# Optimization experiments

Hardware: AMD Instinct MI355X
Metric: run time of the kernel (lower is better)

Reference implementation:

```python
import jax, jax.numpy as jnp
import numpy as np

# longformer-base-4096 config
L, H, D, DH, FF = 12, 12, 768, 64, 3072
B, S, W = 1, 4096, 256            # W = one-sided attention window (attention_window 512)
V, MAXP, NCLS = 50265, 4098, 6
NC = S // W                        # number of chunks of size W


def layer_norm(x, s, b, eps=1e-5):
    m = jnp.mean(x, -1, keepdims=True)
    v = jnp.var(x, -1, keepdims=True)
    return (x - m) * jax.lax.rsqrt(v + eps) * s + b


def sliding_attn(q, k, v, kv_mask):
    # q,k,v: [B,H,S,DH]; kv_mask: [B,S] float (1=keep, 0=pad)
    qc = q.reshape(B, H, NC, W, DH)
    pad = ((0, 0), (0, 0), (W, W), (0, 0))
    kp = jnp.pad(k, pad).reshape(B, H, NC + 2, W, DH)
    vp = jnp.pad(v, pad).reshape(B, H, NC + 2, W, DH)
    # each chunk c sees key chunks c-1, c, c+1 -> [B,H,NC,3W,DH]
    k3 = jnp.concatenate([kp[:, :, i:i + NC] for i in range(3)], axis=3)
    v3 = jnp.concatenate([vp[:, :, i:i + NC] for i in range(3)], axis=3)
    scores = jnp.einsum('bhcqd,bhckd->bhcqk', qc, k3) / np.float32(np.sqrt(DH))
    # banded mask: |key_global - query_global| <= W  <=>  qi <= kj <= qi + 2W
    qi = jnp.arange(W)[:, None]
    kj = jnp.arange(3 * W)[None, :]
    band = (kj >= qi) & (kj <= qi + 2 * W)                       # [W,3W]
    mp = jnp.pad(kv_mask, ((0, 0), (W, W))).reshape(B, NC + 2, W)
    m3 = jnp.concatenate([mp[:, i:i + NC] for i in range(3)], axis=2)  # [B,NC,3W]
    allowed = band[None, None, None] & (m3[:, None, :, None, :] > 0)
    probs = jax.nn.softmax(jnp.where(allowed, scores, -1e9), axis=-1)
    out = jnp.einsum('bhcqk,bhckd->bhcqd', probs, v3)            # [B,H,NC,W,DH]
    return out.reshape(B, H, S, DH)


def setup_inputs():
    ki = iter(jax.random.split(jax.random.key(0), 16))
    p = lambda sh: 0.02 * jax.random.normal(next(ki), sh, jnp.float32)
    ids = jax.random.randint(next(ki), (B, S), 0, V, dtype=jnp.int32)
    mask = jnp.ones((B, S), jnp.int32)
    return dict(
        ids=ids, mask=mask,
        word_emb=p((V, D)), pos_emb=p((MAXP, D)), type_emb=p((D,)),
        ln_e_s=jnp.ones((D,), jnp.float32), ln_e_b=jnp.zeros((D,), jnp.float32),
        wq=p((L, D, D)), bq=jnp.zeros((L, D), jnp.float32),
        wk=p((L, D, D)), bk=jnp.zeros((L, D), jnp.float32),
        wv=p((L, D, D)), bv=jnp.zeros((L, D), jnp.float32),
        wo=p((L, D, D)), bo=jnp.zeros((L, D), jnp.float32),
        ln1_s=jnp.ones((L, D), jnp.float32), ln1_b=jnp.zeros((L, D), jnp.float32),
        w1=p((L, D, FF)), b1=jnp.zeros((L, FF), jnp.float32),
        w2=p((L, FF, D)), b2=jnp.zeros((L, D), jnp.float32),
        ln2_s=jnp.ones((L, D), jnp.float32), ln2_b=jnp.zeros((L, D), jnp.float32),
        w_pool=p((D, D)), b_pool=jnp.zeros((D,), jnp.float32),
        w_cls=p((D, NCLS)), b_cls=jnp.zeros((NCLS,), jnp.float32))


def reference(ids, mask, word_emb, pos_emb, type_emb, ln_e_s, ln_e_b,
              wq, bq, wk, bk, wv, bv, wo, bo, ln1_s, ln1_b,
              w1, b1, w2, b2, ln2_s, ln2_b, w_pool, b_pool, w_cls, b_cls):
    maskf = mask.astype(jnp.float32)
    # RoBERTa-style position ids with padding_idx=1
    pos = (jnp.cumsum(mask, axis=1) * mask + 1).astype(jnp.int32)
    x = word_emb[ids] + pos_emb[pos] + type_emb               # [B,S,D]
    x = layer_norm(x, ln_e_s, ln_e_b)

    def heads(y, w, b):
        return (y @ w + b).reshape(B, S, H, DH).transpose(0, 2, 1, 3)

    for l in range(L):
        q = heads(x, wq[l], bq[l])
        k = heads(x, wk[l], bk[l])
        v = heads(x, wv[l], bv[l])
        a = sliding_attn(q, k, v, maskf)                      # [B,H,S,DH]
        a = a.transpose(0, 2, 1, 3).reshape(B, S, D)
        x = layer_norm(x + (a @ wo[l] + bo[l]), ln1_s[l], ln1_b[l])
        h = jax.nn.gelu(x @ w1[l] + b1[l], approximate=False)
        x = layer_norm(x + (h @ w2[l] + b2[l]), ln2_s[l], ln2_b[l])

    pooled = jnp.tanh(x[:, 0] @ w_pool + b_pool)              # [B,D] pooler
    # Dropout(0.3) is identity in eval mode
    return pooled @ w_cls + b_cls                             # [B,6]
```

## Files before the change

### kernel.cpp

```cpp
#include <hip/hip_runtime.h>
#include <stdint.h>
#include <math.h>

#define NL 12
#define SQ 4096
#define DM 768
#define NH 12
#define DHD 64
#define FF 3072
#define WW 256

typedef unsigned short u16;
typedef __attribute__((ext_vector_type(8))) short bf8_t;
typedef __attribute__((ext_vector_type(4))) short s16x4;
typedef __attribute__((ext_vector_type(4))) float f4;

__device__ __forceinline__ float bf2f(u16 h) {
  union { unsigned int u; float f; } c; c.u = ((unsigned int)h) << 16; return c.f;
}
__device__ __forceinline__ u16 f2bf(float f) {
  union { float f; unsigned int u; } c; c.f = f; unsigned int u = c.u;
  return (u16)((u + 0x7fffu + ((u >> 16) & 1u)) >> 16);
}
__device__ __forceinline__ int iclamp(int v, int lo, int hi) {
  return v < lo ? lo : (v > hi ? hi : v);
}
__device__ __forceinline__ void gload16(const void* g, void* l) {
  __builtin_amdgcn_global_load_lds(
      (const __attribute__((address_space(1))) void*)g,
      (__attribute__((address_space(3))) void*)l, 16, 0, 0);
}

__global__ __launch_bounds__(256) void scan_kernel(const int* __restrict__ mask,
                                                   int* __restrict__ pos) {
  __shared__ int part[256];
  int tid = threadIdx.x;
  int base = tid * 16, ssum = 0;
  for (int i = 0; i < 16; ++i) ssum += mask[base + i];
  part[tid] = ssum;
  __syncthreads();
  if (tid == 0) {
    int run = 0;
    for (int i = 0; i < 256; ++i) { int t = part[i]; part[i] = run; run += t; }
  }
  __syncthreads();
  int run = part[tid];
  for (int i = 0; i < 16; ++i) {
    int m = mask[base + i];
    run += m;
    pos[base + i] = run * m + 1;
  }
}

__device__ __forceinline__ void block_ln4(int row, f4 a, bool act,
    const float* __restrict__ s, const float* __restrict__ b,
    float* __restrict__ xo, u16* __restrict__ xh, float* red, int tid) {
  float s1 = 0.f, s2 = 0.f;
  if (act) {
#pragma unroll
    for (int j = 0; j < 4; ++j) { s1 += a[j]; s2 += a[j] * a[j]; }
  }
#pragma unroll
  for (int m = 1; m < 64; m <<= 1) { s1 += __shfl_xor(s1, m); s2 += __shfl_xor(s2, m); }
  if ((tid & 63) == 0) { red[tid >> 6] = s1; red[4 + (tid >> 6)] = s2; }
  __syncthreads();
  s1 = red[0] + red[1] + red[2] + red[3];
  s2 = red[4] + red[5] + red[6] + red[7];
  float mean = s1 * (1.f / DM);
  float var = s2 * (1.f / DM) - mean * mean;
  float inv = rsqrtf(var + 1e-5f);
  if (act) {
    const f4 sv = ((const f4*)s)[tid];
    const f4 bv = ((const f4*)b)[tid];
    f4 y;
    s16x4 hh;
#pragma unroll
    for (int j = 0; j < 4; ++j) {
      y[j] = (a[j] - mean) * inv * sv[j] + bv[j];
      hh[j] = (short)f2bf(y[j]);
    }
    ((f4*)xo)[(size_t)row * 192 + tid] = y;
    *(s16x4*)&xh[(size_t)row * DM + tid * 4] = hh;
  }
}

__global__ __launch_bounds__(256) void embed_kernel(const int* __restrict__ ids,
    const int* __restrict__ pos, const float* __restrict__ we,
    const float* __restrict__ pe, const float* __restrict__ te,
    const float* __restrict__ s, const float* __restrict__ b,
    float* __restrict__ xo, u16* __restrict__ xh) {
  __shared__ float red[8];
  int row = blockIdx.x, tid = threadIdx.x;
  bool act = tid < 192;
  f4 a = { 0.f, 0.f, 0.f, 0.f };
  if (act) {
    int id = ids[row], pz = pos[row];
    const f4 wv = ((const f4*)we)[(size_t)id * 192 + tid];
    const f4 pv = ((const f4*)pe)[(size_t)pz * 192 + tid];
    const f4 tv = ((const f4*)te)[tid];
#pragma unroll
    for (int j = 0; j < 4; ++j) a[j] = wv[j] + pv[j] + tv[j];
  }
  block_ln4(row, a, act, s, b, xo, xh, red, tid);
}

__global__ __launch_bounds__(256) void ln_direct_kernel(
    const float* __restrict__ in, float* __restrict__ x, u16* __restrict__ xh,
    const float* __restrict__ s, const float* __restrict__ b) {
  __shared__ float red[8];
  int row = blockIdx.x, tid = threadIdx.x;
  bool act = tid < 192;
  f4 a = { 0.f, 0.f, 0.f, 0.f };
  if (act) a = ((const f4*)in)[(size_t)row * 192 + tid];
  block_ln4(row, a, act, s, b, x, xh, red, tid);
}

__global__ __launch_bounds__(256) void ln_fuse_kernel(
    const float* __restrict__ pp, int nparts, const float* __restrict__ bias,
    float* __restrict__ x, u16* __restrict__ xh,
    const float* __restrict__ s, const float* __restrict__ b) {
  __shared__ float red[8];
  int row = blockIdx.x, tid = threadIdx.x;
  bool act = tid < 192;
  f4 a = { 0.f, 0.f, 0.f, 0.f };
  if (act) {
    size_t i4 = (size_t)row * 192 + tid;
    a = ((const f4*)x)[i4];
    const f4 bb = ((const f4*)bias)[tid];
#pragma unroll
    for (int j = 0; j < 4; ++j) a[j] += bb[j];
    for (int p = 0; p < nparts; ++p) {
      const f4 pv = ((const f4*)pp)[(size_t)p * SQ * 192 + i4];
#pragma unroll
      for (int j = 0; j < 4; ++j) a[j] += pv[j];
    }
  }
  block_ln4(row, a, act, s, b, x, xh, red, tid);
}

__global__ __launch_bounds__(256) void wconv_all(
    const float* __restrict__ wq, const float* __restrict__ wk,
    const float* __restrict__ wv, const float* __restrict__ wo,
    const float* __restrict__ w1, const float* __restrict__ w2,
    u16* __restrict__ Wqkv, u16* __restrict__ Wo,
    u16* __restrict__ W1, u16* __restrict__ W2) {
  __shared__ float t[64 * 65];
  int b = blockIdx.x;
  int lay = blockIdx.y;
  const float* src;
  u16* dst;
  int K, N, rowoff, nx, tile;
  if (b < 432) {
    int j = b / 144;
    tile = b - j * 144;
    src = ((j == 0) ? wq : ((j == 1) ? wk : wv)) + (size_t)lay * DM * DM;
    dst = Wqkv + (size_t)lay * 3 * DM * DM;
    K = DM; N = DM; rowoff = j * DM; nx = 12;
  } else if (b < 576) {
    tile = b - 432;
    src = wo + (size_t)lay * DM * DM; dst = Wo + (size_t)lay * DM * DM;
    K = DM; N = DM; rowoff = 0; nx = 12;
  } else if (b < 1152) {
    tile = b - 576;
    src = w1 + (size_t)lay * DM * FF; dst = W1 + (size_t)lay * DM * FF;
    K = DM; N = FF; rowoff = 0; nx = 48;
  } else {
    tile = b - 1152;
    src = w2 + (size_t)lay * FF * DM; dst = W2 + (size_t)lay * FF * DM;
    K = FF; N = DM; rowoff = 0; nx = 12;
  }
  int n0 = (tile % nx) * 64, k0 = (tile / nx) * 64;
  int tid = threadIdx.x;
  int q = tid & 15, kr = tid >> 4;
#pragma unroll
  for (int p = 0; p < 4; ++p) {
    int k = kr + p * 16;
    f4 v = *(const f4*)&src[(size_t)(k0 + k) * N + n0 + q * 4];
#pragma unroll
    for (int j = 0; j < 4; ++j) t[k * 65 + q * 4 + j] = v[j];
  }
  __syncthreads();
  int n = tid >> 4, kq = (tid & 15) * 4;
#pragma unroll
  for (int c = 0; c < 4; ++c) {
    int nn = n + c * 16;
    s16x4 st;
#pragma unroll
    for (int i = 0; i < 4; ++i)
      st[i] = (short)f2bf(t[(kq + i) * 65 + nn]);
    *(s16x4*)&dst[(size_t)(rowoff + n0 + nn) * K + k0 + kq] = st;
  }
}

template <int EPI>
__global__ __launch_bounds__(256, 3) void gemm1(
    const u16* __restrict__ A, const u16* __restrict__ B, int Kld, int ksl,
    int nx, int ntiles,
    const float* __restrict__ bias0, const float* __restrict__ bias1,
    const float* __restrict__ bias2, const float* __restrict__ resid,
    float* __restrict__ outf, u16* __restrict__ oh,
    u16* __restrict__ Qb, u16* __restrict__ Kb, u16* __restrict__ VTb) {
  __shared__ __align__(16) char smem[49152];

  const int tid = threadIdx.x;
  const int l = tid & 63;
  const int w = tid >> 6;
  const int lr = l & 15;
  const int lg = l >> 4;
  const int nwg = gridDim.x;
  const int bid = blockIdx.x;
  const int wg = (bid & 7) * (nwg >> 3) + (bid >> 3);
  const int part = wg / ntiles;
  const int t = wg - part * ntiles;
  const int bm = (t / nx) * 128;
  const int bn = (t % nx) * 64;
  const int k0 = part * ksl;
  const int wr = (w >> 1) * 64;
  const int wc = (w & 1) * 32;

  f4 acc[4][2];
  f4 z = { 0.f, 0.f, 0.f, 0.f };
#pragma unroll
  for (int i = 0; i < 4; ++i)
#pragma unroll
    for (int j = 0; j < 2; ++j) acc[i][j] = z;

  const int srow = tid >> 3;
  const int scol = ((tid & 7) * 8) ^ ((srow & 7) * 8);
  const int xw = (lr & 7) * 8;

  const int nkt = ksl >> 6;

  auto stage = [&](int slot, int kt) {
    int ksrc = k0 + (kt << 6);
    char* la = smem + slot * 24576 + (size_t)(tid & ~63) * 16;
    char* lb = la + 16384;
#pragma unroll
    for (int r = 0; r < 4; ++r)
      gload16(A + (size_t)(bm + srow + r * 32) * Kld + ksrc + scol, la + r * 4096);
#pragma unroll
    for (int r = 0; r < 2; ++r)
      gload16(B + (size_t)(bn + srow + r * 32) * Kld + ksrc + scol, lb + r * 4096);
  };

  stage(0, 0);
  stage(1, 1);
  asm volatile("s_waitcnt vmcnt(6)" ::: "memory");
  __builtin_amdgcn_s_barrier();
  __builtin_amdgcn_sched_barrier(0);

  for (int kt = 0; kt < nkt; ++kt) {
    const int cur = kt & 1;
    const u16* sA = (const u16*)(smem + cur * 24576);
    const u16* sB = sA + 8192;
#pragma unroll
    for (int ks = 0; ks < 2; ++ks) {
      bf8_t af[4], bfr[2];
#pragma unroll
      for (int mt = 0; mt < 4; ++mt)
        af[mt] = *(const bf8_t*)&sA[(wr + mt * 16 + lr) * 64 + ((ks * 32 + lg * 8) ^ xw)];
#pragma unroll
      for (int nt = 0; nt < 2; ++nt)
        bfr[nt] = *(const bf8_t*)&sB[(wc + nt * 16 + lr) * 64 + ((ks * 32 + lg * 8) ^ xw)];
#pragma unroll
      for (int mt = 0; mt < 4; ++mt)
#pragma unroll
        for (int nt = 0; nt < 2; ++nt)
          acc[mt][nt] = __builtin_amdgcn_mfma_f32_16x16x32_bf16(af[mt], bfr[nt], acc[mt][nt], 0, 0, 0);
    }
    asm volatile("s_waitcnt lgkmcnt(0)" ::: "memory");
    __builtin_amdgcn_sched_barrier(0);
    __builtin_amdgcn_s_barrier();
    if (kt + 2 < nkt) {
      stage(cur, kt + 2);
      asm volatile("s_waitcnt vmcnt(6)" ::: "memory");
    } else {
      asm volatile("s_waitcnt vmcnt(0)" ::: "memory");
    }
    __builtin_amdgcn_s_barrier();
    __builtin_amdgcn_sched_barrier(0);
  }
  __syncthreads();

  if constexpr (EPI == 3 || EPI == 4) {
#pragma unroll
    for (int mt = 0; mt < 4; ++mt)
#pragma unroll
      for (int nt = 0; nt < 2; ++nt) {
        int colg = bn + wc + nt * 16 + lr;
#pragma unroll
        for (int r = 0; r < 4; ++r) {
          int rowg = bm + wr + mt * 16 + lg * 4 + r;
          size_t idx = (size_t)rowg * DM + colg;
          if constexpr (EPI == 3) {
            outf[(size_t)part * SQ * DM + idx] = acc[mt][nt][r];
          } else {
            outf[idx] = acc[mt][nt][r] + bias0[colg] + resid[idx];
          }
        }
      }
    return;
  }

  float* ep = (float*)(smem + w * 9216);
  const int nbase = bn + wc;

  if constexpr (EPI == 0) {
    int tgt = nbase / DM;
    int within = nbase - tgt * DM;
    int head = within >> 6;
    const float* bp = (tgt == 0) ? bias0 : ((tgt == 1) ? bias1 : bias2);
    if (tgt == 2) {
#pragma unroll
      for (int mt = 0; mt < 4; ++mt)
#pragma unroll
        for (int nt = 0; nt < 2; ++nt) {
          int dh = (within & 63) + nt * 16 + lr;
          float bb = bp[within + nt * 16 + lr];
          int s0 = bm + wr + mt * 16 + lg * 4;
          s16x4 st;
#pragma unroll
          for (int r = 0; r < 4; ++r) st[r] = (short)f2bf(acc[mt][nt][r] + bb);
          *(s16x4*)&VTb[((size_t)(head * DHD + dh)) * SQ + s0] = st;
        }
    } else {
      u16* dst = (tgt == 0) ? Qb : Kb;
      float scale = (tgt == 0) ? 0.125f : 1.0f;
#pragma unroll
      for (int mt = 0; mt < 4; ++mt)
#pragma unroll
        for (int nt = 0; nt < 2; ++nt)
#pragma unroll
          for (int r = 0; r < 4; ++r)
            ep[(mt * 16 + lg * 4 + r) * 36 + nt * 16 + lr] = acc[mt][nt][r];
      asm volatile("s_waitcnt lgkmcnt(0)" ::: "memory");
      int coloff = (l & 7) * 4;
#pragma unroll
      for (int i = 0; i < 8; ++i) {
        int row = (l >> 3) + i * 8;
        int gs = bm + wr + row;
        f4 v = *(f4*)&ep[row * 36 + coloff];
        s16x4 st;
#pragma unroll
        for (int j = 0; j < 4; ++j)
          st[j] = (short)f2bf((v[j] + bp[within + coloff + j]) * scale);
        *(s16x4*)&dst[((size_t)head * SQ + gs) * DHD + (within & 63) + coloff] = st;
      }
    }
  } else {
#pragma unroll
    for (int mt = 0; mt < 4; ++mt)
#pragma unroll
      for (int nt = 0; nt < 2; ++nt)
#pragma unroll
        for (int r = 0; r < 4; ++r)
          ep[(mt * 16 + lg * 4 + r) * 36 + nt * 16 + lr] = acc[mt][nt][r];
    asm volatile("s_waitcnt lgkmcnt(0)" ::: "memory");
    int coloff = (l & 7) * 4;
#pragma unroll
    for (int i = 0; i < 8; ++i) {
      int row = (l >> 3) + i * 8;
      int gs = bm + wr + row;
      f4 v = *(f4*)&ep[row * 36 + coloff];
      s16x4 hi;
#pragma unroll
      for (int j = 0; j < 4; ++j) {
        float t2 = v[j] + bias0[nbase + coloff + j];
        t2 = 0.5f * t2 * (1.f + erff(t2 * 0.70710678118654752f));
        hi[j] = (short)f2bf(t2);
      }
      *(s16x4*)&oh[(size_t)gs * FF + nbase + coloff] = hi;
    }
  }
}

__global__ __launch_bounds__(64) void attn_kernel(
    const u16* __restrict__ Qb, const u16* __restrict__ Kb,
    const u16* __restrict__ VTb, const int* __restrict__ mask,
    u16* __restrict__ ah) {
  __shared__ __align__(16) u16 Pl[64 * 72];
  __shared__ float mwin[576];
  const int l = threadIdx.x;
  const int lr = l & 15, lg = l >> 4;
  const int h = blockIdx.y;
  const int q0 = blockIdx.x * 64;
  const int kb = q0 - 256;
  for (int i = l; i < 576; i += 64) {
    int kg = kb + i;
    mwin[i] = (kg >= 0 && kg < SQ && mask[kg] != 0) ? 1.f : 0.f;
  }
  __syncthreads();

  bf8_t qf[4][2];
#pragma unroll
  for (int mt = 0; mt < 4; ++mt)
#pragma unroll
    for (int ks = 0; ks < 2; ++ks)
      qf[mt][ks] = *(const bf8_t*)&Qb[((size_t)h * SQ + q0 + mt * 16 + lr) * DHD + ks * 32 + lg * 8];

  f4 o[4][4];
  f4 z = { 0.f, 0.f, 0.f, 0.f };
  float mrow[4][4], lrow[4][4];
#pragma unroll
  for (int mt = 0; mt < 4; ++mt)
#pragma unroll
    for (int nt = 0; nt < 4; ++nt) o[mt][nt] = z;
#pragma unroll
  for (int mt = 0; mt < 4; ++mt)
#pragma unroll
    for (int r = 0; r < 4; ++r) { mrow[mt][r] = -1e30f; lrow[mt][r] = 0.f; }

  for (int kc = 0; kc < 9; ++kc) {
    int klb = kc * 64;
    f4 sc[4][4];
#pragma unroll
    for (int mt = 0; mt < 4; ++mt)
#pragma unroll
      for (int nt = 0; nt < 4; ++nt) sc[mt][nt] = z;
#pragma unroll
    for (int ks = 0; ks < 2; ++ks) {
      bf8_t kf[4];
#pragma unroll
      for (int nt = 0; nt < 4; ++nt) {
        int krow = iclamp(kb + klb + nt * 16 + lr, 0, SQ - 1);
        kf[nt] = *(const bf8_t*)&Kb[((size_t)h * SQ + krow) * DHD + ks * 32 + lg * 8];
      }
#pragma unroll
      for (int mt = 0; mt < 4; ++mt)
#pragma unroll
        for (int nt = 0; nt < 4; ++nt)
          sc[mt][nt] = __builtin_amdgcn_mfma_f32_16x16x32_bf16(qf[mt][ks], kf[nt], sc[mt][nt], 0, 0, 0);
    }
    bool edge = (kc == 0) | (kc == 8);
#pragma unroll
    for (int mt = 0; mt < 4; ++mt)
#pragma unroll
      for (int nt = 0; nt < 4; ++nt) {
        int col = nt * 16 + lr;
        int kg = kb + klb + col;
        float mk = mwin[klb + col];
#pragma unroll
        for (int r = 0; r < 4; ++r) {
          int qg = q0 + mt * 16 + lg * 4 + r;
          int d = kg - qg;
          bool ok = (mk > 0.5f) && (!edge || ((d <= WW) && (d >= -WW)));
          sc[mt][nt][r] = ok ? sc[mt][nt][r] : -3.0e38f;
        }
      }
#pragma unroll
    for (int mt = 0; mt < 4; ++mt)
#pragma unroll
      for (int r = 0; r < 4; ++r) {
        float cm = fmaxf(fmaxf(sc[mt][0][r], sc[mt][1][r]),
                         fmaxf(sc[mt][2][r], sc[mt][3][r]));
#pragma unroll
        for (int m2 = 1; m2 < 16; m2 <<= 1) cm = fmaxf(cm, __shfl_xor(cm, m2));
        float mn = fmaxf(fmaxf(mrow[mt][r], cm), -1e30f);
        float scl = __expf(mrow[mt][r] - mn);
        mrow[mt][r] = mn;
        float ps = 0.f;
#pragma unroll
        for (int nt = 0; nt < 4; ++nt) {
          float pv = __expf(sc[mt][nt][r] - mn);
          sc[mt][nt][r] = pv;
          ps += pv;
        }
#pragma unroll
        for (int m2 = 1; m2 < 16; m2 <<= 1) ps += __shfl_xor(ps, m2);
        lrow[mt][r] = lrow[mt][r] * scl + ps;
#pragma unroll
        for (int nt = 0; nt < 4; ++nt) o[mt][nt][r] *= scl;
#pragma unroll
        for (int nt = 0; nt < 4; ++nt)
          Pl[(mt * 16 + lg * 4 + r) * 72 + nt * 16 + lr] = f2bf(sc[mt][nt][r]);
      }
    asm volatile("s_waitcnt lgkmcnt(0)" ::: "memory");
#pragma unroll
    for (int ks = 0; ks < 2; ++ks) {
      bf8_t pa[4], vf[4];
#pragma unroll
      for (int mt = 0; mt < 4; ++mt)
        pa[mt] = *(const bf8_t*)&Pl[(mt * 16 + lr) * 72 + ks * 32 + lg * 8];
      int kbase = iclamp(kb + klb + ks * 32 + lg * 8, 0, SQ - 8);
#pragma unroll
      for (int nt = 0; nt < 4; ++nt)
        vf[nt] = *(const bf8_t*)&VTb[((size_t)h * DHD + nt * 16 + lr) * SQ + kbase];
#pragma unroll
      for (int mt = 0; mt < 4; ++mt)
#pragma unroll
        for (int nt = 0; nt < 4; ++nt)
          o[mt][nt] = __builtin_amdgcn_mfma_f32_16x16x32_bf16(pa[mt], vf[nt], o[mt][nt], 0, 0, 0);
    }
  }
#pragma unroll
  for (int mt = 0; mt < 4; ++mt)
#pragma unroll
    for (int nt = 0; nt < 4; ++nt) {
      int col = h * DHD + nt * 16 + lr;
#pragma unroll
      for (int r = 0; r < 4; ++r) {
        int gq = q0 + mt * 16 + lg * 4 + r;
        float v = o[mt][nt][r] / lrow[mt][r];
        ah[(size_t)gq * DM + col] = f2bf(v);
      }
    }
}

__global__ __launch_bounds__(256) void head1_kernel(const float* __restrict__ x,
    const float* __restrict__ wp, const float* __restrict__ bp,
    float* __restrict__ y) {
  __shared__ float x0[DM];
  __shared__ float part[4][64];
  int tid = threadIdx.x;
  int w = tid >> 6, l = tid & 63;
  for (int i = tid; i < DM; i += 256) x0[i] = x[i];
  __syncthreads();
  int j = blockIdx.x * 64 + l;
  float a = 0.f;
  int i0 = w * 192;
#pragma unroll 4
  for (int i = i0; i < i0 + 192; ++i) a += x0[i] * wp[(size_t)i * DM + j];
  part[w][l] = a;
  __syncthreads();
  if (w == 0) {
    float t = part[0][l] + part[1][l] + part[2][l] + part[3][l] + bp[j];
    y[j] = tanhf(t);
  }
}

__global__ __launch_bounds__(64) void head2_kernel(const float* __restrict__ y,
    const float* __restrict__ wc, const float* __restrict__ bc,
    float* __restrict__ out) {
  int l = threadIdx.x;
  float acc[6] = {0.f, 0.f, 0.f, 0.f, 0.f, 0.f};
  for (int i = l; i < DM; i += 64) {
    float yv = y[i];
#pragma unroll
    for (int j = 0; j < 6; ++j) acc[j] += yv * wc[i * 6 + j];
  }
#pragma unroll
  for (int j = 0; j < 6; ++j)
#pragma unroll
    for (int m = 1; m < 64; m <<= 1) acc[j] += __shfl_xor(acc[j], m);
  if (l == 0) {
#pragma unroll
    for (int j = 0; j < 6; ++j) out[j] = acc[j] + bc[j];
  }
}

extern "C" void kernel_launch(void* const* d_in, const int* in_sizes, int n_in,
                              void* d_out, int out_size, void* d_ws, size_t ws_size,
                              hipStream_t stream) {
  const int* ids = (const int*)d_in[0];
  const int* mask = (const int*)d_in[1];
  const float* we = (const float*)d_in[2];
  const float* pe = (const float*)d_in[3];
  const float* te = (const float*)d_in[4];
  const float* ln_e_s = (const float*)d_in[5];
  const float* ln_e_b = (const float*)d_in[6];
  const float* wq = (const float*)d_in[7];
  const float* bq = (const float*)d_in[8];
  const float* wk = (const float*)d_in[9];
  const float* bk = (const float*)d_in[10];
  const float* wv = (const float*)d_in[11];
  const float* bv = (const float*)d_in[12];
  const float* wo = (const float*)d_in[13];
  const float* bo = (const float*)d_in[14];
  const float* ln1_s = (const float*)d_in[15];
  const float* ln1_b = (const float*)d_in[16];
  const float* w1 = (const float*)d_in[17];
  const float* b1 = (const float*)d_in[18];
  const float* w2 = (const float*)d_in[19];
  const float* b2 = (const float*)d_in[20];
  const float* ln2_s = (const float*)d_in[21];
  const float* ln2_b = (const float*)d_in[22];
  const float* wpool = (const float*)d_in[23];
  const float* bpool = (const float*)d_in[24];
  const float* wcls = (const float*)d_in[25];
  const float* bcls = (const float*)d_in[26];

  char* p = (char*)d_ws;
  auto take = [&](size_t bytes) {
    char* r = p;
    p += (bytes + 255) & ~(size_t)255;
    return r;
  };
  int* pos = (int*)take((size_t)SQ * 4);
  float* x = (float*)take((size_t)SQ * DM * 4);
  float* pp = (float*)take((size_t)2 * SQ * DM * 4);
  u16* xh = (u16*)take((size_t)SQ * DM * 2);
  u16* Wqkv_h = (u16*)take((size_t)NL * 3 * DM * DM * 2);
  u16* Wo_h = (u16*)take((size_t)NL * DM * DM * 2);
  u16* W1_h = (u16*)take((size_t)NL * DM * FF * 2);
  u16* W2_h = (u16*)take((size_t)NL * FF * DM * 2);
  u16* Qb = (u16*)take((size_t)NH * SQ * DHD * 2);
  u16* Kbf = (u16*)take((size_t)NH * SQ * DHD * 2);
  u16* VTb = (u16*)take((size_t)NH * DHD * SQ * 2);
  u16* ah_ = (u16*)take((size_t)SQ * DM * 2);
  u16* hh = (u16*)take((size_t)SQ * FF * 2);
  float* ypool = (float*)take((size_t)DM * 4);

  scan_kernel<<<dim3(1), dim3(256), 0, stream>>>(mask, pos);
  embed_kernel<<<dim3(SQ), dim3(256), 0, stream>>>(ids, pos, we, pe, te, ln_e_s, ln_e_b, x, xh);
  wconv_all<<<dim3(1728, NL), dim3(256), 0, stream>>>(
      wq, wk, wv, wo, w1, w2, Wqkv_h, Wo_h, W1_h, W2_h);

  for (int l = 0; l < NL; ++l) {
    const u16* Wq_l = Wqkv_h + (size_t)l * 3 * DM * DM;
    const u16* Wo_l = Wo_h + (size_t)l * DM * DM;
    const u16* W1_l = W1_h + (size_t)l * DM * FF;
    const u16* W2_l = W2_h + (size_t)l * FF * DM;

    gemm1<0><<<dim3(1152), dim3(256), 0, stream>>>(
        xh, Wq_l, DM, DM, 36, 1152, bq + (size_t)l * DM, bk + (size_t)l * DM,
        bv + (size_t)l * DM, nullptr, nullptr, nullptr, Qb, Kbf, VTb);
    attn_kernel<<<dim3(SQ / 64, NH), dim3(64), 0, stream>>>(Qb, Kbf, VTb, mask, ah_);
    gemm1<4><<<dim3(384), dim3(256), 0, stream>>>(
        ah_, Wo_l, DM, DM, 12, 384, bo + (size_t)l * DM, nullptr, nullptr, x,
        pp, nullptr, nullptr, nullptr, nullptr);
    ln_direct_kernel<<<dim3(SQ), dim3(256), 0, stream>>>(
        pp, x, xh, ln1_s + (size_t)l * DM, ln1_b + (size_t)l * DM);
    gemm1<2><<<dim3(1536), dim3(256), 0, stream>>>(
        xh, W1_l, DM, DM, 48, 1536, b1 + (size_t)l * FF, nullptr, nullptr, nullptr,
        nullptr, hh, nullptr, nullptr, nullptr);
    gemm1<3><<<dim3(768), dim3(256), 0, stream>>>(
        hh, W2_l, FF, FF / 2, 12, 384, nullptr, nullptr, nullptr, nullptr,
        pp, nullptr, nullptr, nullptr, nullptr);
    ln_fuse_kernel<<<dim3(SQ), dim3(256), 0, stream>>>(
        pp, 2, b2 + (size_t)l * DM, x, xh, ln2_s + (size_t)l * DM, ln2_b + (size_t)l * DM);
  }

  head1_kernel<<<dim3(12), dim3(256), 0, stream>>>(x, wpool, bpool, ypool);
  head2_kernel<<<dim3(1), dim3(64), 0, stream>>>(ypool, wcls, bcls, (float*)d_out);
}
```

Before: 2.241 ms.

## Split attention key chunks across two waves with flash-style merge

The attention kernel now runs two wavefronts per 64-query block. Each wave processes about half of the nine 64-key chunks with its own online softmax, and the partial max, sum and output are then merged through shared memory. It also precomputes per-chunk mask sums so that interior chunks with no padding skip the masking pass. The goal is more parallelism and latency hiding for the attention step, at the cost of extra shared memory, two barriers and the merge work.

```diff
diff --git a/kernel.cpp b/kernel.cpp
--- a/kernel.cpp
+++ b/kernel.cpp
@@ -374,22 +374,34 @@
   }
 }
 
-__global__ __launch_bounds__(64) void attn_kernel(
+__global__ __launch_bounds__(128) void attn_kernel(
     const u16* __restrict__ Qb, const u16* __restrict__ Kb,
     const u16* __restrict__ VTb, const int* __restrict__ mask,
     u16* __restrict__ ah) {
-  __shared__ __align__(16) u16 Pl[64 * 72];
+  __shared__ __align__(16) char sbuf[18432];
   __shared__ float mwin[576];
-  const int l = threadIdx.x;
+  __shared__ float allm[9];
+  __shared__ float mpart[2][64], lpart[2][64];
+  const int tid = threadIdx.x;
+  const int w = tid >> 6;
+  const int l = tid & 63;
   const int lr = l & 15, lg = l >> 4;
   const int h = blockIdx.y;
   const int q0 = blockIdx.x * 64;
   const int kb = q0 - 256;
-  for (int i = l; i < 576; i += 64) {
+  u16* Plw = (u16*)(sbuf + (size_t)w * 9216);
+
+  for (int i = tid; i < 576; i += 128) {
     int kg = kb + i;
     mwin[i] = (kg >= 0 && kg < SQ && mask[kg] != 0) ? 1.f : 0.f;
   }
   __syncthreads();
+  if (tid < 9) {
+    float s = 0.f;
+#pragma unroll 8
+    for (int i = 0; i < 64; ++i) s += mwin[tid * 64 + i];
+    allm[tid] = s;
+  }
 
   bf8_t qf[4][2];
 #pragma unroll
@@ -409,8 +421,11 @@
   for (int mt = 0; mt < 4; ++mt)
 #pragma unroll
     for (int r = 0; r < 4; ++r) { mrow[mt][r] = -1e30f; lrow[mt][r] = 0.f; }
-
-  for (int kc = 0; kc < 9; ++kc) {
+  __syncthreads();
+
+  const int kcb = w * 5;
+  const int kce = kcb + 5 - w;
+  for (int kc = kcb; kc < kce; ++kc) {
     int klb = kc * 64;
     f4 sc[4][4];
 #pragma unroll
@@ -432,21 +447,23 @@
           sc[mt][nt] = __builtin_amdgcn_mfma_f32_16x16x32_bf16(qf[mt][ks], kf[nt], sc[mt][nt], 0, 0, 0);
     }
     bool edge = (kc == 0) | (kc == 8);
-#pragma unroll
-    for (int mt = 0; mt < 4; ++mt)
-#pragma unroll
-      for (int nt = 0; nt < 4; ++nt) {
-        int col = nt * 16 + lr;
-        int kg = kb + klb + col;
-        float mk = mwin[klb + col];
-#pragma unroll
-        for (int r = 0; r < 4; ++r) {
-          int qg = q0 + mt * 16 + lg * 4 + r;
-          int d = kg - qg;
-          bool ok = (mk > 0.5f) && (!edge || ((d <= WW) && (d >= -WW)));
-          sc[mt][nt][r] = ok ? sc[mt][nt][r] : -3.0e38f;
+    if (edge || allm[kc] < 63.5f) {
+#pragma unroll
+      for (int mt = 0; mt < 4; ++mt)
+#pragma unroll
+        for (int nt = 0; nt < 4; ++nt) {
+          int col = nt * 16 + lr;
+          int kg = kb + klb + col;
+          float mk = mwin[klb + col];
+#pragma unroll
+          for (int r = 0; r < 4; ++r) {
+            int qg = q0 + mt * 16 + lg * 4 + r;
+            int d = kg - qg;
+            bool ok = (mk > 0.5f) && (!edge || ((d <= WW) && (d >= -WW)));
+            sc[mt][nt][r] = ok ? sc[mt][nt][r] : -3.0e38f;
+          }
         }
-      }
+    }
 #pragma unroll
     for (int mt = 0; mt < 4; ++mt)
 #pragma unroll
@@ -472,7 +489,7 @@
         for (int nt = 0; nt < 4; ++nt) o[mt][nt][r] *= scl;
 #pragma unroll
         for (int nt = 0; nt < 4; ++nt)
-          Pl[(mt * 16 + lg * 4 + r) * 72 + nt * 16 + lr] = f2bf(sc[mt][nt][r]);
+          Plw[(mt * 16 + lg * 4 + r) * 72 + nt * 16 + lr] = f2bf(sc[mt][nt][r]);
       }
     asm volatile("s_waitcnt lgkmcnt(0)" ::: "memory");
 #pragma unroll
@@ -480,7 +497,7 @@
       bf8_t pa[4], vf[4];
 #pragma unroll
       for (int mt = 0; mt < 4; ++mt)
-        pa[mt] = *(const bf8_t*)&Pl[(mt * 16 + lr) * 72 + ks * 32 + lg * 8];
+        pa[mt] = *(const bf8_t*)&Plw[(mt * 16 + lr) * 72 + ks * 32 + lg * 8];
       int kbase = iclamp(kb + klb + ks * 32 + lg * 8, 0, SQ - 8);
 #pragma unroll
       for (int nt = 0; nt < 4; ++nt)
@@ -492,18 +509,57 @@
           o[mt][nt] = __builtin_amdgcn_mfma_f32_16x16x32_bf16(pa[mt], vf[nt], o[mt][nt], 0, 0, 0);
     }
   }
+
+  if (lr == 0) {
+#pragma unroll
+    for (int mt = 0; mt < 4; ++mt)
+#pragma unroll
+      for (int r = 0; r < 4; ++r) {
+        int row = mt * 16 + lg * 4 + r;
+        mpart[w][row] = mrow[mt][r];
+        lpart[w][row] = lrow[mt][r];
+      }
+  }
+  __syncthreads();
+  float* oacc = (float*)sbuf;
 #pragma unroll
   for (int mt = 0; mt < 4; ++mt)
 #pragma unroll
-    for (int nt = 0; nt < 4; ++nt) {
-      int col = h * DHD + nt * 16 + lr;
-#pragma unroll
-      for (int r = 0; r < 4; ++r) {
-        int gq = q0 + mt * 16 + lg * 4 + r;
-        float v = o[mt][nt][r] / lrow[mt][r];
-        ah[(size_t)gq * DM + col] = f2bf(v);
-      }
-    }
+    for (int r = 0; r < 4; ++r) {
+      int row = mt * 16 + lg * 4 + r;
+      float m0 = mpart[0][row], m1 = mpart[1][row];
+      float mf = fmaxf(m0, m1);
+      float sw = __expf(mrow[mt][r] - mf);
+#pragma unroll
+      for (int nt = 0; nt < 4; ++nt) o[mt][nt][r] *= sw;
+      lrow[mt][r] = lpart[0][row] * __expf(m0 - mf) + lpart[1][row] * __expf(m1 - mf);
+    }
+  if (w == 1) {
+#pragma unroll
+    for (int mt = 0; mt < 4; ++mt)
+#pragma unroll
+      for (int nt = 0; nt < 4; ++nt) {
+        int col = nt * 16 + lr;
+#pragma unroll
+        for (int r = 0; r < 4; ++r)
+          oacc[(mt * 16 + lg * 4 + r) * 68 + col] = o[mt][nt][r];
+      }
+  }
+  __syncthreads();
+  if (w == 0) {
+#pragma unroll
+    for (int mt = 0; mt < 4; ++mt)
+#pragma unroll
+      for (int nt = 0; nt < 4; ++nt) {
+        int col = h * DHD + nt * 16 + lr;
+#pragma unroll
+        for (int r = 0; r < 4; ++r) {
+          int row = mt * 16 + lg * 4 + r;
+          float v = (o[mt][nt][r] + oacc[row * 68 + nt * 16 + lr]) / lrow[mt][r];
+          ah[(size_t)(q0 + row) * DM + col] = f2bf(v);
+        }
+      }
+  }
 }
 
 __global__ __launch_bounds__(256) void head1_kernel(const float* __restrict__ x,
@@ -614,7 +670,7 @@
     gemm1<0><<<dim3(1152), dim3(256), 0, stream>>>(
         xh, Wq_l, DM, DM, 36, 1152, bq + (size_t)l * DM, bk + (size_t)l * DM,
         bv + (size_t)l * DM, nullptr, nullptr, nullptr, Qb, Kbf, VTb);
-    attn_kernel<<<dim3(SQ / 64, NH), dim3(64), 0, stream>>>(Qb, Kbf, VTb, mask, ah_);
+    attn_kernel<<<dim3(SQ / 64, NH), dim3(128), 0, stream>>>(Qb, Kbf, VTb, mask, ah_);
     gemm1<4><<<dim3(384), dim3(256), 0, stream>>>(
         ah_, Wo_l, DM, DM, 12, 384, bo + (size_t)l * DM, nullptr, nullptr, x,
         pp, nullptr, nullptr, nullptr, nullptr);
```

Result: slower. 2.405 ms (+7.3%).
